# Performance work log

Measured on AMD Instinct MI355X. Metric: run time of the kernel, lower is better.

Reference implementation:

```python
import jax, jax.numpy as jnp
import numpy as np

V = 50257  # vocab_size
H = 512    # d_model
S = 512    # source length
B = 8      # batch
T = 64     # decode steps


def setup_inputs() -> dict:
    key = jax.random.key(0)
    k1, k2, k3, k4, k5, k6 = jax.random.split(key, 6)
    src_full = jax.random.randint(k1, (S, B), 0, V, dtype=jnp.int32)
    decode_output = jax.random.normal(k2, (T, B, H), dtype=jnp.float32)
    decode_attn = jax.random.uniform(k3, (B, T, S), dtype=jnp.float32)
    memory = jax.random.normal(k4, (S, B, H), dtype=jnp.float32)
    # learned params: gen_proj (H->V) and prob_proj (H->1)
    W_gen = jax.random.normal(k5, (H, V), dtype=jnp.float32) / np.sqrt(H)
    b_gen = jnp.zeros((V,), dtype=jnp.float32)
    W_prob = jax.random.normal(k6, (H, 1), dtype=jnp.float32) / np.sqrt(H)
    b_prob = jnp.zeros((1,), dtype=jnp.float32)
    return {
        "src_full": src_full,
        "decode_output": decode_output,
        "decode_attn": decode_attn,
        "memory": memory,
        "W_gen": W_gen,
        "b_gen": b_gen,
        "W_prob": W_prob,
        "b_prob": b_prob,
    }


def reference(src_full, decode_output, decode_attn, memory, W_gen, b_gen, W_prob, b_prob):
    # context[t,b,h] = sum_s attn[b,t,s] * memory[s,b,h]
    context = jnp.einsum("bts,sbh->tbh", decode_attn, memory)  # [T,B,H]
    prob = jax.nn.sigmoid(context @ W_prob + b_prob)           # [T,B,1] copy gate p_gen
    gen_logits = prob * jax.nn.softmax(decode_output @ W_gen + b_gen, axis=-1)  # [T,B,V]

    # scatter-add attention mass onto vocab slots: copy[t,b, src_full[s,b]] += attn[b,t,s]
    attn_tbs = jnp.transpose(decode_attn, (1, 0, 2))  # [T,B,S]
    idx = src_full.T                                  # [B,S]
    ti = jnp.arange(T)[:, None, None]
    bi = jnp.arange(B)[None, :, None]
    copy_logits = jnp.zeros((T, B, V), dtype=decode_attn.dtype).at[ti, bi, idx[None, :, :]].add(attn_tbs)
    copy_logits = (1.0 - prob) * jax.nn.softmax(copy_logits, axis=-1)

    return jnp.log(gen_logits + copy_logits)
```

## Files before the change

kernel.cpp:

```cpp
#include <hip/hip_runtime.h>
#include <hip/hip_bf16.h>
#include <math.h>

#define VV 50257
#define VP 50304
#define HH 512
#define SS 512
#define BB 8
#define TT 64
#define MM (TT*BB)

typedef __bf16 bf16x2 __attribute__((ext_vector_type(2)));
typedef __bf16 bf16x4 __attribute__((ext_vector_type(4)));
typedef __bf16 bf16x8 __attribute__((ext_vector_type(8)));
typedef float  f32x4  __attribute__((ext_vector_type(4)));

__device__ __forceinline__ __bf16 f2b(float f) {
    unsigned u = __builtin_bit_cast(unsigned, f);
    unsigned r = (u + 0x7fffu + ((u >> 16) & 1u)) >> 16;
    unsigned short s = (unsigned short)r;
    return __builtin_bit_cast(__bf16, s);
}

__device__ __forceinline__ void gl2lds16(const void* g, void* l) {
    __builtin_amdgcn_global_load_lds(
        (const __attribute__((address_space(1))) unsigned*)g,
        (__attribute__((address_space(3))) unsigned*)l, 16, 0, 0);
}

#define WAITV(n) asm volatile("s_waitcnt vmcnt(" #n ")" ::: "memory")

__global__ __launch_bounds__(256) void k_pre(const float* __restrict__ A,
                                             __bf16* __restrict__ Ab,
                                             const float* __restrict__ mem,
                                             const float* __restrict__ Wp,
                                             float* __restrict__ mw) {
    int tid = threadIdx.x;
    if (blockIdx.x < 256) {
        int i = (blockIdx.x * 256 + tid) * 4;
        float4 v = *(const float4*)&A[i];
        bf16x4 o = {f2b(v.x), f2b(v.y), f2b(v.z), f2b(v.w)};
        *(bf16x4*)&Ab[i] = o;
    } else {
        int bx = blockIdx.x - 256;
        int row = bx * 4 + (tid >> 6);
        int lane = tid & 63;
        const float* mp = mem + (size_t)row * HH;
        float acc = 0.f;
#pragma unroll
        for (int i = 0; i < HH / 64; i++)
            acc += mp[lane + 64 * i] * Wp[lane + 64 * i];
#pragma unroll
        for (int off = 32; off > 0; off >>= 1) acc += __shfl_down(acc, off);
        if (lane == 0) mw[row] = acc;
    }
}

__global__ __launch_bounds__(256) void k_wt(const float* __restrict__ W,
                                            __bf16* __restrict__ Wt,
                                            const float* __restrict__ attn,
                                            const float* __restrict__ mw,
                                            const float* __restrict__ bp,
                                            float* __restrict__ prob,
                                            float* __restrict__ Z) {
    __shared__ float tile[32][33];
    __shared__ __bf16 Wo[32][520];
    int tid = threadIdx.x;

    if (blockIdx.x < VP / 32) {
        int n0 = blockIdx.x * 32;
        int nn = tid >> 3, ks = (tid & 7) * 4;
        for (int kc = 0; kc < 16; kc++) {
            int k0 = kc * 32;
#pragma unroll
            for (int rd = 0; rd < 4; rd++) {
                int idx = rd * 256 + tid;
                int kk = idx >> 5, nc = idx & 31;
                int n = n0 + nc;
                tile[kk][nc] = (n < VV) ? W[(size_t)(k0 + kk) * VV + n] : 0.f;
            }
            __syncthreads();
            bf16x4 o = {f2b(tile[ks][nn]), f2b(tile[ks + 1][nn]),
                        f2b(tile[ks + 2][nn]), f2b(tile[ks + 3][nn])};
            *(bf16x4*)&Wo[nn][k0 + ks] = o;
            __syncthreads();
        }
#pragma unroll
        for (int i = 0; i < 8; i++) {
            int r = i * 4 + (tid >> 6);
            int c = (tid & 63) * 8;
            *(bf16x8*)&Wt[(size_t)(n0 + r) * HH + c] = *(const bf16x8*)&Wo[r][c];
        }
    } else {
        int r = blockIdx.x - VP / 32;
        int t = r / BB, b = r % BB;
        const float* ap = attn + ((size_t)b * TT + t) * SS;
        float acc = ap[tid] * mw[tid * BB + b] +
                    ap[tid + 256] * mw[(tid + 256) * BB + b];
        float* red = &tile[0][0];
        red[tid] = acc; __syncthreads();
        for (int st = 128; st > 0; st >>= 1) {
            if (tid < st) red[tid] += red[tid + st];
            __syncthreads();
        }
        if (tid == 0) {
            prob[r] = 1.f / (1.f + expf(-(red[0] + bp[0])));
            Z[r] = 0.f;
        }
    }
}

template<bool BF16OUT>
__global__ __launch_bounds__(512, 6) void k_gemm5(const __bf16* __restrict__ Ab,
                                                  const __bf16* __restrict__ Wt,
                                                  const float* __restrict__ bias,
                                                  float* __restrict__ Cf,
                                                  __bf16* __restrict__ Cb,
                                                  float* __restrict__ Zrow) {
    __shared__ __bf16 As[3][4096];
    __shared__ __bf16 Bs[3][4096];
    __shared__ float zred[128];

    const int tid  = threadIdx.x;
    const int lane = tid & 63;
    const int wave = tid >> 6;
    const int l15  = lane & 15;
    const int quad = lane >> 4;
    const int wr = (wave >> 2) * 64;
    const int wc = (wave & 3) * 32;

    int L = blockIdx.x + gridDim.x * blockIdx.y;
    int xcd = L & 7, i8 = L >> 3;
    int nid = (xcd < 4 ? xcd * 197 : 4 * 197 + (xcd - 4) * 196) + i8;
    const int row0 = (nid & 3) * 128;
    const int col0 = (nid >> 2) * 128;

    const size_t offA = (size_t)(row0 + wave * 16 + l15) * HH + quad * 8;
    const size_t offB = (size_t)(col0 + wave * 16 + l15) * HH + quad * 8;

#define STAGE(buf, k0)                                    \
    do {                                                  \
        gl2lds16(Ab + offA + (k0), &As[buf][wave * 512]); \
        gl2lds16(Wt + offB + (k0), &Bs[buf][wave * 512]); \
    } while (0)

    f32x4 acc[4][2] = {};

    STAGE(0, 0);
    STAGE(1, 32);
#pragma unroll
    for (int it = 0; it < 16; ++it) {
        if (it < 15) WAITV(2);
        else         WAITV(0);
        __builtin_amdgcn_s_barrier();
        if (it < 14) STAGE((it + 2) % 3, (it + 2) * 32);
        const __bf16* Al = &As[it % 3][0];
        const __bf16* Bl = &Bs[it % 3][0];
        bf16x8 af[4], bfv[2];
#pragma unroll
        for (int mt = 0; mt < 4; mt++)
            af[mt] = *(const bf16x8*)&Al[((wr >> 4) + mt) * 512 + lane * 8];
#pragma unroll
        for (int nt = 0; nt < 2; nt++)
            bfv[nt] = *(const bf16x8*)&Bl[((wc >> 4) + nt) * 512 + lane * 8];
        __builtin_amdgcn_s_setprio(1);
#pragma unroll
        for (int mt = 0; mt < 4; mt++)
#pragma unroll
            for (int nt = 0; nt < 2; nt++)
                acc[mt][nt] = __builtin_amdgcn_mfma_f32_16x16x32_bf16(
                    af[mt], bfv[nt], acc[mt][nt], 0, 0, 0);
        __builtin_amdgcn_s_setprio(0);
    }
#undef STAGE

    __syncthreads();
    if (tid < 128) zred[tid] = 0.f;
    __syncthreads();

#pragma unroll
    for (int mt = 0; mt < 4; mt++) {
        float esum[4] = {0.f, 0.f, 0.f, 0.f};
#pragma unroll
        for (int nt = 0; nt < 2; nt++) {
            int c = col0 + wc + nt * 16 + l15;
            if (c < VV) {
                float bv = bias[c];
#pragma unroll
                for (int i = 0; i < 4; i++) {
                    int r = row0 + wr + mt * 16 + quad * 4 + i;
                    float l = acc[mt][nt][i] + bv;
                    if (BF16OUT) Cb[(size_t)r * VP + c] = f2b(l);
                    else         Cf[(size_t)r * VV + c] = l;
                    esum[i] += __expf(l);
                }
            }
        }
#pragma unroll
        for (int i = 0; i < 4; i++) {
            float e = esum[i];
            e += __shfl_xor(e, 1);
            e += __shfl_xor(e, 2);
            e += __shfl_xor(e, 4);
            e += __shfl_xor(e, 8);
            if (l15 == 0)
                atomicAdd(&zred[wr + mt * 16 + quad * 4 + i], e);
        }
    }
    __syncthreads();
    if (tid < 128) atomicAdd(&Zrow[row0 + tid], zred[tid]);
}

#define HT 1024
#define NBW 1572

__device__ __forceinline__ void build_hash(const int* __restrict__ src,
                                           const float* __restrict__ ap,
                                           int b, int tid,
                                           int* keys, float* vals, unsigned* bmap,
                                           float* red, int* s_D, float* s_Zc) {
    for (int i = tid; i < HT; i += 256) { keys[i] = -1; vals[i] = 0.f; }
    for (int i = tid; i < NBW; i += 256) bmap[i] = 0u;
    if (tid == 0) *s_D = 0;
    __syncthreads();

    for (int s = tid; s < SS; s += 256) {
        int idx = src[s * BB + b];
        float v = ap[s];
        unsigned h = ((unsigned)idx * 2654435761u) >> 22;
        while (true) {
            int old = atomicCAS(&keys[h], -1, idx);
            if (old == -1 || old == idx) { atomicAdd(&vals[h], v); break; }
            h = (h + 1) & (HT - 1);
        }
    }
    __syncthreads();

    float lsum = 0.f; int dloc = 0;
    for (int i = tid; i < HT; i += 256) {
        int k = keys[i];
        if (k != -1) {
            lsum += __expf(vals[i]); dloc++;
            atomicOr(&bmap[(unsigned)k >> 5], 1u << (k & 31));
        }
    }
    atomicAdd(s_D, dloc);
    red[tid] = lsum; __syncthreads();
    for (int st = 128; st > 0; st >>= 1) {
        if (tid < st) red[tid] += red[tid + st];
        __syncthreads();
    }
    if (tid == 0) *s_Zc = (float)(VV - *s_D) + red[0];
    __syncthreads();
}

#define HV (VP / 2)
__global__ __launch_bounds__(1024) void k_final2(const int* __restrict__ src,
                                                 const float* __restrict__ attn,
                                                 const float* __restrict__ prob,
                                                 const float* __restrict__ Zrow,
                                                 const __bf16* __restrict__ LG,
                                                 float* __restrict__ out) {
    __shared__ int      keys[HT];
    __shared__ float    vals[HT];
    __shared__ unsigned bmap[NBW];
    __shared__ float    red[1024];
    __shared__ int      s_D;
    __shared__ float    s_Zc;

    int r = blockIdx.y;
    int half = blockIdx.x;
    int t = r / BB, b = r % BB;
    int tid = threadIdx.x;
    const float* ap = attn + ((size_t)b * TT + t) * SS;

    { keys[tid] = -1; vals[tid] = 0.f; }
    for (int i = tid; i < NBW; i += 1024) bmap[i] = 0u;
    if (tid == 0) s_D = 0;
    __syncthreads();

    if (tid < SS) {
        int idx = src[tid * BB + b];
        float v = ap[tid];
        unsigned h = ((unsigned)idx * 2654435761u) >> 22;
        while (true) {
            int old = atomicCAS(&keys[h], -1, idx);
            if (old == -1 || old == idx) { atomicAdd(&vals[h], v); break; }
            h = (h + 1) & (HT - 1);
        }
    }
    __syncthreads();

    float lsum = 0.f;
    {
        int k = keys[tid];
        bool occ = (k != -1);
        if (occ) {
            lsum = __expf(vals[tid]);
            atomicOr(&bmap[(unsigned)k >> 5], 1u << (k & 31));
        }
        unsigned long long m = __ballot(occ);
        if ((tid & 63) == 0) atomicAdd(&s_D, __popcll(m));
    }
    red[tid] = lsum; __syncthreads();
    for (int st = 512; st > 0; st >>= 1) {
        if (tid < st) red[tid] += red[tid + st];
        __syncthreads();
    }
    if (tid == 0) s_Zc = (float)(VV - s_D) + red[0];
    __syncthreads();

    float p = prob[r];
    float pinvZ = p / Zrow[r];
    float qinvZc = (1.f - p) / s_Zc;

    const __bf16* lrow = LG + (size_t)r * VP;
    float* orow = out + (size_t)r * VV;

    int base = half * HV;
    for (int v0 = base + tid * 8; v0 < base + HV; v0 += 8192) {
        bf16x8 l8 = *(const bf16x8*)&lrow[v0];
        unsigned bits = (bmap[v0 >> 5] >> (v0 & 31)) & 0xFFu;
        if (bits == 0u && v0 + 8 <= VV) {
#pragma unroll
            for (int e = 0; e < 8; e++)
                orow[v0 + e] = __logf(pinvZ * __expf((float)l8[e]) + qinvZc);
        } else {
#pragma unroll
            for (int e = 0; e < 8; e++) {
                int v = v0 + e;
                if (v < VV) {
                    float l = (float)l8[e];
                    float c = 1.f;
                    if ((bits >> e) & 1u) {
                        unsigned h = ((unsigned)v * 2654435761u) >> 22;
                        while (true) {
                            int k = keys[h];
                            if (k == v) { c = __expf(vals[h]); break; }
                            if (k == -1) break;
                            h = (h + 1) & (HT - 1);
                        }
                    }
                    orow[v] = __logf(pinvZ * __expf(l) + qinvZc * c);
                }
            }
        }
    }
}

#define CHUNKS 6283
__global__ __launch_bounds__(256) void k_final_s(const int* __restrict__ src,
                                                 const float* __restrict__ attn,
                                                 const float* __restrict__ prob,
                                                 const float* __restrict__ Zrow,
                                                 float* __restrict__ out) {
    __shared__ int      keys[HT];
    __shared__ float    vals[HT];
    __shared__ unsigned bmap[NBW];
    __shared__ float    red[256];
    __shared__ int      s_D;
    __shared__ float    s_Zc;

    int r = blockIdx.y;
    int t = r / BB, b = r % BB;
    int tid = threadIdx.x;
    const float* ap = attn + ((size_t)b * TT + t) * SS;
    build_hash(src, ap, b, tid, keys, vals, bmap, red, &s_D, &s_Zc);

    float p = prob[r];
    float pinvZ = p / Zrow[r];
    float qinvZc = (1.f - p) / s_Zc;

    int c0 = blockIdx.x * CHUNKS;
    int c1 = c0 + CHUNKS; if (c1 > VV) c1 = VV;
    float* rowp = out + (size_t)r * VV;

    for (int v = c0 + tid; v < c1; v += 256) {
        float l = rowp[v];
        float c = 1.f;
        if ((bmap[v >> 5] >> (v & 31)) & 1u) {
            unsigned h = ((unsigned)v * 2654435761u) >> 22;
            while (true) {
                int k = keys[h];
                if (k == v) { c = __expf(vals[h]); break; }
                if (k == -1) break;
                h = (h + 1) & (HT - 1);
            }
        }
        rowp[v] = __logf(pinvZ * __expf(l) + qinvZc * c);
    }
}

extern "C" void kernel_launch(void* const* d_in, const int* in_sizes, int n_in,
                              void* d_out, int out_size, void* d_ws, size_t ws_size,
                              hipStream_t stream) {
    const int*   src_full      = (const int*)d_in[0];
    const float* decode_output = (const float*)d_in[1];
    const float* decode_attn   = (const float*)d_in[2];
    const float* memory        = (const float*)d_in[3];
    const float* W_gen         = (const float*)d_in[4];
    const float* b_gen         = (const float*)d_in[5];
    const float* W_prob        = (const float*)d_in[6];
    const float* b_prob        = (const float*)d_in[7];
    float* out = (float*)d_out;

    float* ws   = (float*)d_ws;
    float* mw   = ws;
    float* prob = ws + 4096;
    float* Z    = ws + 4608;
    __bf16* Ab  = (__bf16*)(ws + 5120);
    __bf16* Wt  = (__bf16*)(ws + 5120 + 131072);
    __bf16* LG  = Wt + (size_t)VP * HH;

    size_t base_b = (size_t)(5120 + 131072) * sizeof(float);
    size_t wt_b   = (size_t)VP * HH * 2;
    size_t lg_b   = (size_t)MM * VP * 2;
    bool full = ws_size >= base_b + wt_b + lg_b;

    k_pre<<<1280, 256, 0, stream>>>(decode_output, Ab, memory, W_prob, mw);
    k_wt<<<VP / 32 + 512, 256, 0, stream>>>(W_gen, Wt, decode_attn, mw, b_prob,
                                            prob, Z);

    dim3 ggrid(MM / 128, VP / 128);
    if (full) {
        k_gemm5<true><<<ggrid, 512, 0, stream>>>(Ab, Wt, b_gen, nullptr, LG, Z);
        dim3 fgrid(2, MM);
        k_final2<<<fgrid, 1024, 0, stream>>>(src_full, decode_attn, prob, Z, LG, out);
    } else {
        k_gemm5<false><<<ggrid, 512, 0, stream>>>(Ab, Wt, b_gen, out, nullptr, Z);
        dim3 fgrid((VV + CHUNKS - 1) / CHUNKS, MM);
        k_final_s<<<fgrid, 256, 0, stream>>>(src_full, decode_attn, prob, Z, out);
    }
}
```

Baseline: 328.9 us.

## Enlarge GEMM block tile to 256x128 and double-buffer W transpose tiles

The GEMM block tile grows from 128x128 to 256x128, with each wave computing a 64x64 sub-tile, which halves the number of column blocks along M and lets each B tile be reused across twice as many rows. The XCD-aware block remapping and the launch bounds change to match (occupancy hint from 6 to 4). The W transpose kernel now ping-pongs between two tiles and drops the per-iteration second barrier, aiming to cut sync overhead. In exchange the GEMM uses more registers and LDS per block and launches half as many blocks.

```diff
diff --git a/kernel.cpp b/kernel.cpp
--- a/kernel.cpp
+++ b/kernel.cpp
@@ -30,11 +30,11 @@
 
 #define WAITV(n) asm volatile("s_waitcnt vmcnt(" #n ")" ::: "memory")
 
-__global__ __launch_bounds__(256) void k_pre(const float* __restrict__ A,
-                                             __bf16* __restrict__ Ab,
-                                             const float* __restrict__ mem,
-                                             const float* __restrict__ Wp,
-                                             float* __restrict__ mw) {
+__global__ __launch_bounds__(256) void k_pre0(const float* __restrict__ A,
+                                              __bf16* __restrict__ Ab,
+                                              const float* __restrict__ mem,
+                                              const float* __restrict__ Wp,
+                                              float* __restrict__ mw) {
     int tid = threadIdx.x;
     if (blockIdx.x < 256) {
         int i = (blockIdx.x * 256 + tid) * 4;
@@ -56,35 +56,38 @@
     }
 }
 
-__global__ __launch_bounds__(256) void k_wt(const float* __restrict__ W,
-                                            __bf16* __restrict__ Wt,
-                                            const float* __restrict__ attn,
-                                            const float* __restrict__ mw,
-                                            const float* __restrict__ bp,
-                                            float* __restrict__ prob,
-                                            float* __restrict__ Z) {
-    __shared__ float tile[32][33];
+#define NWT (VP / 32)
+__global__ __launch_bounds__(256) void k_wt2(const float* __restrict__ W,
+                                             __bf16* __restrict__ Wt,
+                                             const float* __restrict__ attn,
+                                             const float* __restrict__ mw,
+                                             const float* __restrict__ bp,
+                                             float* __restrict__ prob,
+                                             float* __restrict__ Z) {
+    __shared__ float tile[2][32][33];
     __shared__ __bf16 Wo[32][520];
     int tid = threadIdx.x;
 
-    if (blockIdx.x < VP / 32) {
+    if (blockIdx.x < NWT) {
         int n0 = blockIdx.x * 32;
         int nn = tid >> 3, ks = (tid & 7) * 4;
+#pragma unroll
         for (int kc = 0; kc < 16; kc++) {
             int k0 = kc * 32;
+            int p = kc & 1;
 #pragma unroll
             for (int rd = 0; rd < 4; rd++) {
                 int idx = rd * 256 + tid;
                 int kk = idx >> 5, nc = idx & 31;
                 int n = n0 + nc;
-                tile[kk][nc] = (n < VV) ? W[(size_t)(k0 + kk) * VV + n] : 0.f;
+                tile[p][kk][nc] = (n < VV) ? W[(size_t)(k0 + kk) * VV + n] : 0.f;
             }
             __syncthreads();
-            bf16x4 o = {f2b(tile[ks][nn]), f2b(tile[ks + 1][nn]),
-                        f2b(tile[ks + 2][nn]), f2b(tile[ks + 3][nn])};
+            bf16x4 o = {f2b(tile[p][ks][nn]), f2b(tile[p][ks + 1][nn]),
+                        f2b(tile[p][ks + 2][nn]), f2b(tile[p][ks + 3][nn])};
             *(bf16x4*)&Wo[nn][k0 + ks] = o;
-            __syncthreads();
-        }
+        }
+        __syncthreads();
 #pragma unroll
         for (int i = 0; i < 8; i++) {
             int r = i * 4 + (tid >> 6);
@@ -92,12 +95,12 @@
             *(bf16x8*)&Wt[(size_t)(n0 + r) * HH + c] = *(const bf16x8*)&Wo[r][c];
         }
     } else {
-        int r = blockIdx.x - VP / 32;
+        int r = blockIdx.x - NWT;
         int t = r / BB, b = r % BB;
         const float* ap = attn + ((size_t)b * TT + t) * SS;
         float acc = ap[tid] * mw[tid * BB + b] +
                     ap[tid + 256] * mw[(tid + 256) * BB + b];
-        float* red = &tile[0][0];
+        float* red = &tile[0][0][0];
         red[tid] = acc; __syncthreads();
         for (int st = 128; st > 0; st >>= 1) {
             if (tid < st) red[tid] += red[tid + st];
@@ -111,63 +114,67 @@
 }
 
 template<bool BF16OUT>
-__global__ __launch_bounds__(512, 6) void k_gemm5(const __bf16* __restrict__ Ab,
+__global__ __launch_bounds__(512, 4) void k_gemm6(const __bf16* __restrict__ Ab,
                                                   const __bf16* __restrict__ Wt,
                                                   const float* __restrict__ bias,
                                                   float* __restrict__ Cf,
                                                   __bf16* __restrict__ Cb,
                                                   float* __restrict__ Zrow) {
-    __shared__ __bf16 As[3][4096];
+    __shared__ __bf16 As[3][8192];
     __shared__ __bf16 Bs[3][4096];
-    __shared__ float zred[128];
+    __shared__ float zred[256];
 
     const int tid  = threadIdx.x;
     const int lane = tid & 63;
     const int wave = tid >> 6;
     const int l15  = lane & 15;
     const int quad = lane >> 4;
-    const int wr = (wave >> 2) * 64;
-    const int wc = (wave & 3) * 32;
+    const int wr = (wave >> 1) * 64;
+    const int wc = (wave & 1) * 64;
 
     int L = blockIdx.x + gridDim.x * blockIdx.y;
     int xcd = L & 7, i8 = L >> 3;
-    int nid = (xcd < 4 ? xcd * 197 : 4 * 197 + (xcd - 4) * 196) + i8;
-    const int row0 = (nid & 3) * 128;
-    const int col0 = (nid >> 2) * 128;
-
-    const size_t offA = (size_t)(row0 + wave * 16 + l15) * HH + quad * 8;
+    int nid = (xcd < 2 ? xcd * 99 : 2 * 99 + (xcd - 2) * 98) + i8;
+    const int row0 = (nid & 1) * 256;
+    const int col0 = (nid >> 1) * 128;
+
+    size_t offA[2];
+#pragma unroll
+    for (int q = 0; q < 2; q++)
+        offA[q] = (size_t)(row0 + (2 * wave + q) * 16 + l15) * HH + quad * 8;
     const size_t offB = (size_t)(col0 + wave * 16 + l15) * HH + quad * 8;
 
-#define STAGE(buf, k0)                                    \
-    do {                                                  \
-        gl2lds16(Ab + offA + (k0), &As[buf][wave * 512]); \
-        gl2lds16(Wt + offB + (k0), &Bs[buf][wave * 512]); \
+#define STAGE(buf, k0)                                                       \
+    do {                                                                     \
+        gl2lds16(Ab + offA[0] + (k0), &As[buf][(2 * wave) * 512]);           \
+        gl2lds16(Ab + offA[1] + (k0), &As[buf][(2 * wave + 1) * 512]);       \
+        gl2lds16(Wt + offB + (k0),    &Bs[buf][wave * 512]);                 \
     } while (0)
 
-    f32x4 acc[4][2] = {};
+    f32x4 acc[4][4] = {};
 
     STAGE(0, 0);
     STAGE(1, 32);
 #pragma unroll
     for (int it = 0; it < 16; ++it) {
-        if (it < 15) WAITV(2);
+        if (it < 15) WAITV(3);
         else         WAITV(0);
         __builtin_amdgcn_s_barrier();
         if (it < 14) STAGE((it + 2) % 3, (it + 2) * 32);
         const __bf16* Al = &As[it % 3][0];
         const __bf16* Bl = &Bs[it % 3][0];
-        bf16x8 af[4], bfv[2];
+        bf16x8 af[4], bfv[4];
 #pragma unroll
         for (int mt = 0; mt < 4; mt++)
             af[mt] = *(const bf16x8*)&Al[((wr >> 4) + mt) * 512 + lane * 8];
 #pragma unroll
-        for (int nt = 0; nt < 2; nt++)
+        for (int nt = 0; nt < 4; nt++)
             bfv[nt] = *(const bf16x8*)&Bl[((wc >> 4) + nt) * 512 + lane * 8];
         __builtin_amdgcn_s_setprio(1);
 #pragma unroll
         for (int mt = 0; mt < 4; mt++)
 #pragma unroll
-            for (int nt = 0; nt < 2; nt++)
+            for (int nt = 0; nt < 4; nt++)
                 acc[mt][nt] = __builtin_amdgcn_mfma_f32_16x16x32_bf16(
                     af[mt], bfv[nt], acc[mt][nt], 0, 0, 0);
         __builtin_amdgcn_s_setprio(0);
@@ -175,14 +182,14 @@
 #undef STAGE
 
     __syncthreads();
-    if (tid < 128) zred[tid] = 0.f;
+    if (tid < 256) zred[tid] = 0.f;
     __syncthreads();
 
 #pragma unroll
     for (int mt = 0; mt < 4; mt++) {
         float esum[4] = {0.f, 0.f, 0.f, 0.f};
 #pragma unroll
-        for (int nt = 0; nt < 2; nt++) {
+        for (int nt = 0; nt < 4; nt++) {
             int c = col0 + wc + nt * 16 + l15;
             if (c < VV) {
                 float bv = bias[c];
@@ -208,7 +215,7 @@
         }
     }
     __syncthreads();
-    if (tid < 128) atomicAdd(&Zrow[row0 + tid], zred[tid]);
+    if (tid < 256) atomicAdd(&Zrow[row0 + tid], zred[tid]);
 }
 
 #define HT 1024
@@ -417,17 +424,17 @@
     size_t lg_b   = (size_t)MM * VP * 2;
     bool full = ws_size >= base_b + wt_b + lg_b;
 
-    k_pre<<<1280, 256, 0, stream>>>(decode_output, Ab, memory, W_prob, mw);
-    k_wt<<<VP / 32 + 512, 256, 0, stream>>>(W_gen, Wt, decode_attn, mw, b_prob,
-                                            prob, Z);
-
-    dim3 ggrid(MM / 128, VP / 128);
+    k_pre0<<<1280, 256, 0, stream>>>(decode_output, Ab, memory, W_prob, mw);
+    k_wt2<<<NWT + 512, 256, 0, stream>>>(W_gen, Wt, decode_attn, mw, b_prob,
+                                         prob, Z);
+
+    dim3 ggrid(MM / 256, VP / 128);
     if (full) {
-        k_gemm5<true><<<ggrid, 512, 0, stream>>>(Ab, Wt, b_gen, nullptr, LG, Z);
+        k_gemm6<true><<<ggrid, 512, 0, stream>>>(Ab, Wt, b_gen, nullptr, LG, Z);
         dim3 fgrid(2, MM);
         k_final2<<<fgrid, 1024, 0, stream>>>(src_full, decode_attn, prob, Z, LG, out);
     } else {
-        k_gemm5<false><<<ggrid, 512, 0, stream>>>(Ab, Wt, b_gen, out, nullptr, Z);
+        k_gemm6<false><<<ggrid, 512, 0, stream>>>(Ab, Wt, b_gen, out, nullptr, Z);
         dim3 fgrid((VV + CHUNKS - 1) / CHUNKS, MM);
         k_final_s<<<fgrid, 256, 0, stream>>>(src_full, decode_attn, prob, Z, out);
     }
```

New measurement: 359.0 us. 1.09x slower.
